# Kernel tuning notes

Hardware: AMD Instinct MI355X
Metric: run time of the kernel (lower is better)

Reference implementation:

```python
import jax, jax.numpy as jnp
import numpy as np

MAX_K = 4
KAPPA_MAX = 80.0
TEMP = 0.7

NPOINT1, NSAMPLE1 = 128, 32
NPOINT2, NSAMPLE2 = 32, 32


def _sqdist(a, b):
    # a: (B,M,3), b: (B,N,3) -> (B,M,N) squared euclidean distance
    return (jnp.sum(a * a, -1)[:, :, None] + jnp.sum(b * b, -1)[:, None, :]
            - 2.0 * jnp.einsum('bmc,bnc->bmn', a, b))


def _fps(xyz, npoint):
    # farthest point sampling, sequential over npoint (inherent recurrence)
    B, N, _ = xyz.shape
    def step(carry, _):
        dist, far = carry
        centroid = jnp.take_along_axis(xyz, far[:, None, None], axis=1)  # (B,1,3)
        d = jnp.sum((xyz - centroid) ** 2, -1)                            # (B,N)
        dist = jnp.minimum(dist, d)
        nxt = jnp.argmax(dist, -1).astype(jnp.int32)
        return (dist, nxt), far
    init = (jnp.full((B, N), 1e10, xyz.dtype), jnp.zeros((B,), jnp.int32))
    _, idx = jax.lax.scan(step, init, None, length=npoint)
    return jnp.transpose(idx)  # (B, npoint)


def _gather(x, idx):
    # x: (B,N,C), idx: (B,...) int -> (B,...,C)
    return jax.vmap(lambda xb, ib: xb[ib])(x, idx)


def _sa(xyz, feats, npoint, nsample, params, group_all=False):
    # PointNet++ set abstraction: FPS + kNN grouping + shared MLP + max-pool
    if group_all:
        new_xyz = jnp.zeros((xyz.shape[0], 1, 3), xyz.dtype)
        g = xyz[:, None]                                   # (B,1,N,3)
        if feats is not None:
            g = jnp.concatenate([g, feats[:, None]], -1)   # (B,1,N,3+C)
    else:
        fidx = _fps(xyz, npoint)                           # (B,S)
        new_xyz = _gather(xyz, fidx)                       # (B,S,3)
        d = _sqdist(new_xyz, xyz)                          # (B,S,N)
        _, nidx = jax.lax.top_k(-d, nsample)               # (B,S,K) nearest
        g = _gather(xyz, nidx) - new_xyz[:, :, None]       # relative coords
        if feats is not None:
            g = jnp.concatenate([g, _gather(feats, nidx)], -1)
    for w, b in params:                                    # shared 1x1 MLP
        g = jax.nn.relu(g @ w + b)
    return new_xyz, jnp.max(g, axis=2)                     # max over group


def _ln(x, g, b, eps=1e-5):
    m = jnp.mean(x, -1, keepdims=True)
    v = jnp.var(x, -1, keepdims=True)
    return (x - m) * jax.lax.rsqrt(v + eps) * g + b


def setup_inputs() -> dict:
    key = jax.random.key(0)
    ks = iter(jax.random.split(key, 64))
    def p(shape, s=0.05):
        return jax.random.normal(next(ks), shape, jnp.float32) * s
    d = {"xyz": jax.random.normal(next(ks), (32, 16384, 3), jnp.float32)}
    sa_dims = {"sa1": [3, 64, 64, 128], "sa2": [131, 128, 128, 256], "sa3": [259, 256, 512, 1024]}
    for name, dims in sa_dims.items():
        for i in range(3):
            d[f"{name}_w{i}"] = p((dims[i], dims[i + 1]))
            d[f"{name}_b{i}"] = jnp.zeros((dims[i + 1],), jnp.float32)
    d["fc1_w"] = p((1024, 512)); d["fc1_b"] = jnp.zeros((512,), jnp.float32)
    d["ln1_g"] = jnp.ones((512,), jnp.float32); d["ln1_b"] = jnp.zeros((512,), jnp.float32)
    d["fc2_w"] = p((512, 256)); d["fc2_b"] = jnp.zeros((256,), jnp.float32)
    d["ln2_g"] = jnp.ones((256,), jnp.float32); d["ln2_b"] = jnp.zeros((256,), jnp.float32)
    d["pi_w"] = p((256, MAX_K)); d["pi_b"] = jnp.zeros((MAX_K,), jnp.float32)
    d["mu_w"] = p((256, MAX_K * 2)); d["mu_b"] = jnp.zeros((MAX_K * 2,), jnp.float32)
    d["kappa_w"] = p((256, MAX_K)); d["kappa_b"] = jnp.zeros((MAX_K,), jnp.float32)
    return d


def reference(xyz,
              sa1_w0, sa1_b0, sa1_w1, sa1_b1, sa1_w2, sa1_b2,
              sa2_w0, sa2_b0, sa2_w1, sa2_b1, sa2_w2, sa2_b2,
              sa3_w0, sa3_b0, sa3_w1, sa3_b1, sa3_w2, sa3_b2,
              fc1_w, fc1_b, ln1_g, ln1_b, fc2_w, fc2_b, ln2_g, ln2_b,
              pi_w, pi_b, mu_w, mu_b, kappa_w, kappa_b):
    l1x, l1f = _sa(xyz, None, NPOINT1, NSAMPLE1,
                   [(sa1_w0, sa1_b0), (sa1_w1, sa1_b1), (sa1_w2, sa1_b2)])
    l2x, l2f = _sa(l1x, l1f, NPOINT2, NSAMPLE2,
                   [(sa2_w0, sa2_b0), (sa2_w1, sa2_b1), (sa2_w2, sa2_b2)])
    _, l3f = _sa(l2x, l2f, None, None,
                 [(sa3_w0, sa3_b0), (sa3_w1, sa3_b1), (sa3_w2, sa3_b2)], group_all=True)
    x = l3f.reshape(l3f.shape[0], -1)  # (B,1024)
    x = jax.nn.relu(_ln(x @ fc1_w + fc1_b, ln1_g, ln1_b))  # dropout is identity in eval
    x = jax.nn.relu(_ln(x @ fc2_w + fc2_b, ln2_g, ln2_b))
    weight = jax.nn.softmax((x @ pi_w + pi_b) / TEMP, axis=-1)
    mu_raw = (x @ mu_w + mu_b).reshape(-1, MAX_K, 2)
    nrm = jnp.linalg.norm(mu_raw, axis=-1, keepdims=True)
    mu_unit = mu_raw / jnp.maximum(nrm, 1e-4)              # F.normalize(eps=1e-4)
    c, s = mu_unit[..., 0], mu_unit[..., 1]
    n2 = jnp.sqrt(c * c + s * s)
    mask = n2 < 1e-3
    c = jnp.where(mask, 1.0, c)
    s = jnp.where(mask, 0.0, s)
    mu = jnp.arctan2(s, c)
    kappa = jnp.minimum(jax.nn.softplus(x @ kappa_w + kappa_b) + 1e-6, KAPPA_MAX)
    return mu, kappa, weight
```

## Files before the change

### kernel.cpp

```cpp
#include <hip/hip_runtime.h>
#include <math.h>

#define B 32
#define N1 16384
#define NP1 128
#define NS1 32
#define NP2 32
#define NS2 32

#define OFF_L1X   0
#define OFF_G1    12288
#define OFF_L1F   405504
#define OFF_L2X   929792
#define OFF_NIDX2 932864
#define OFF_L2F   965632
#define OFF_L3F   1227776

__global__ __launch_bounds__(1024, 1) void k_fps1(const float* __restrict__ xyz,
                                                  float* __restrict__ l1x) {
  const int b = blockIdx.x, t = threadIdx.x;
  const float* xb = xyz + (size_t)b * N1 * 3;
  float px[16], py[16], pz[16], dd[16];
#pragma unroll
  for (int j = 0; j < 16; ++j) {
    int idx = t + (j << 10);
    px[j] = xb[idx * 3 + 0]; py[j] = xb[idx * 3 + 1]; pz[j] = xb[idx * 3 + 2];
    dd[j] = 1e10f;
  }
#pragma unroll
  for (int j = 0; j < 16; ++j) {
    asm volatile("" : "+v"(px[j]), "+v"(py[j]), "+v"(pz[j]));
  }
  __shared__ unsigned long long slots[2][16];
  if (t < 16) slots[0][t] = (t == 0) ? 0xFFFFFFFFull : 0ull;
  __syncthreads();
  for (int it = 0; it < NP1; ++it) {
    unsigned long long key = slots[it & 1][0];
#pragma unroll
    for (int w = 1; w < 16; ++w) {
      unsigned long long k2 = slots[it & 1][w];
      if (k2 > key) key = k2;
    }
    const int widx = (int)(0xFFFFFFFFu - (unsigned)(key & 0xFFFFFFFFull));
    const float cx = xb[widx * 3 + 0];
    const float cy = xb[widx * 3 + 1];
    const float cz = xb[widx * 3 + 2];
    if (t == 0) {
      float* o = l1x + ((size_t)b * NP1 + it) * 3;
      o[0] = cx; o[1] = cy; o[2] = cz;
    }
    float bd = -1.f; int bj = 0;
#pragma unroll
    for (int j = 0; j < 16; ++j) {
      float dx = px[j] - cx, dy = py[j] - cy, dz = pz[j] - cz;
      float d = dx * dx + dy * dy + dz * dz;
      float nd = fminf(dd[j], d);
      dd[j] = nd;
      if (nd > bd) { bd = nd; bj = j; }
    }
    unsigned long long mykey =
        ((unsigned long long)__float_as_uint(bd) << 32) |
        (unsigned long long)(0xFFFFFFFFu - (unsigned)(t + (bj << 10)));
#pragma unroll
    for (int off = 32; off > 0; off >>= 1) {
      unsigned long long ok = __shfl_down(mykey, off);
      if (ok > mykey) mykey = ok;
    }
    if ((t & 63) == 0) slots[(it + 1) & 1][t >> 6] = mykey;
    __syncthreads();
  }
}

__device__ __forceinline__ float dist3(const float* __restrict__ xb, int idx,
                                       float cx, float cy, float cz,
                                       float& x, float& y, float& z) {
  x = xb[idx * 3 + 0]; y = xb[idx * 3 + 1]; z = xb[idx * 3 + 2];
  float dx = x - cx, dy = y - cy, dz = z - cz;
  return dx * dx + dy * dy + dz * dz;
}

#define KNN_CAP 512
#define NBIN 2048

__global__ __launch_bounds__(256) void k_knn1(const float* __restrict__ xyz,
                                              const float* __restrict__ l1x,
                                              float* __restrict__ g1) {
  const int t = threadIdx.x;
  const int b = blockIdx.x & 31;
  const int m = blockIdx.x >> 5;
  const float* xb = xyz + (size_t)b * N1 * 3;
  const float* cp = l1x + ((size_t)b * NP1 + m) * 3;
  const float cx = cp[0], cy = cp[1], cz = cp[2];

  __shared__ int hist[NBIN];
  __shared__ float cd[KNN_CAP]; __shared__ int ci[KNN_CAP];
  __shared__ float cpx[KNN_CAP], cpy[KNN_CAP], cpz[KNN_CAP];
  __shared__ int s_cnt, s_cut;
  __shared__ int wsum[4];

  for (int i = t; i < NBIN; i += 256) hist[i] = 0;
  if (t == 0) { s_cnt = 0; s_cut = NBIN - 1; }
  __syncthreads();

  for (int j = 0; j < 64; ++j) {
    float x, y, z;
    float d = dist3(xb, t + (j << 8), cx, cy, cz, x, y, z);
    atomicAdd(&hist[__float_as_uint(d) >> 20], 1);
  }
  __syncthreads();

  {
    int loc = 0;
#pragma unroll
    for (int j = 0; j < 8; ++j) loc += hist[t * 8 + j];
    int v = loc;
#pragma unroll
    for (int off = 1; off < 64; off <<= 1) {
      int u = __shfl_up(v, off);
      if ((t & 63) >= off) v += u;
    }
    if ((t & 63) == 63) wsum[t >> 6] = v;
    __syncthreads();
    int woff = 0;
    for (int w = 0; w < (t >> 6); ++w) woff += wsum[w];
    int incl = v + woff, excl = incl - loc;
    if (excl < NS1 && incl >= NS1) {
      int c = excl;
#pragma unroll
      for (int j = 0; j < 8; ++j) {
        c += hist[t * 8 + j];
        if (c >= NS1) { s_cut = t * 8 + j; break; }
      }
    }
  }
  __syncthreads();
  const unsigned cut = (unsigned)s_cut + 1u;

  for (int j = 0; j < 64; ++j) {
    float x, y, z;
    float d = dist3(xb, t + (j << 8), cx, cy, cz, x, y, z);
    if ((__float_as_uint(d) >> 20) <= cut) {
      int p = atomicAdd(&s_cnt, 1);
      if (p < KNN_CAP) { cd[p] = d; ci[p] = t + (j << 8); cpx[p] = x; cpy[p] = y; cpz[p] = z; }
    }
  }
  __syncthreads();
  const int cnt = (s_cnt < KNN_CAP) ? s_cnt : KNN_CAP;

  float* gout = g1 + ((size_t)(b * NP1 + m)) * NS1 * 3;
  for (int p = t; p < cnt; p += 256) {
    const float dp = cd[p]; const int ip = ci[p];
    int rank = 0;
    for (int q = 0; q < cnt; ++q) {
      float dq = cd[q];
      rank += (dq < dp || (dq == dp && ci[q] < ip)) ? 1 : 0;
    }
    if (rank < NS1) {
      gout[rank * 3 + 0] = cpx[p] - cx;
      gout[rank * 3 + 1] = cpy[p] - cy;
      gout[rank * 3 + 2] = cpz[p] - cz;
    }
  }
}

template <int K, int C, int TPT>
__device__ __forceinline__ void sa_layer(const float* __restrict__ W,
                                         const float* __restrict__ bias,
                                         const float* __restrict__ hin, int instride,
                                         float* __restrict__ hout,
                                         unsigned* __restrict__ om,
                                         float* __restrict__ wst, int t) {
  constexpr int CT = C / 4;
  constexpr int NT = 8 * CT;
  float acc[TPT][4][4];
  int s4[TPT], c4[TPT]; bool on[TPT];
#pragma unroll
  for (int p = 0; p < TPT; ++p) {
    int tile = t + p * 256;
    on[p] = tile < NT;
    int tl = on[p] ? tile : 0;
    s4[p] = (tl / CT) * 4; c4[p] = (tl % CT) * 4;
    float4 bb = *(const float4*)(bias + c4[p]);
#pragma unroll
    for (int i = 0; i < 4; ++i) {
      acc[p][i][0] = bb.x; acc[p][i][1] = bb.y; acc[p][i][2] = bb.z; acc[p][i][3] = bb.w;
    }
  }
  for (int k0 = 0; k0 < K; k0 += 16) {
    const int kc = (K - k0 < 16) ? (K - k0) : 16;
    __syncthreads();
    for (int i = t; i < kc * C; i += 256) wst[i] = W[k0 * C + i];
    __syncthreads();
    if (kc == 16) {
#pragma unroll
      for (int kk = 0; kk < 16; ++kk) {
#pragma unroll
        for (int p = 0; p < TPT; ++p) {
          float4 w = *(const float4*)(wst + kk * C + c4[p]);
#pragma unroll
          for (int i = 0; i < 4; ++i) {
            float a = hin[(s4[p] + i) * instride + (k0 + kk)];
            acc[p][i][0] += a * w.x; acc[p][i][1] += a * w.y;
            acc[p][i][2] += a * w.z; acc[p][i][3] += a * w.w;
          }
        }
      }
    } else {
      for (int kk = 0; kk < kc; ++kk) {
#pragma unroll
        for (int p = 0; p < TPT; ++p) {
          float4 w = *(const float4*)(wst + kk * C + c4[p]);
#pragma unroll
          for (int i = 0; i < 4; ++i) {
            float a = hin[(s4[p] + i) * instride + (k0 + kk)];
            acc[p][i][0] += a * w.x; acc[p][i][1] += a * w.y;
            acc[p][i][2] += a * w.z; acc[p][i][3] += a * w.w;
          }
        }
      }
    }
  }
#pragma unroll
  for (int p = 0; p < TPT; ++p) {
    if (!on[p]) continue;
    if (om) {
#pragma unroll
      for (int j = 0; j < 4; ++j) {
        float vm = fmaxf(fmaxf(fmaxf(acc[p][0][j], acc[p][1][j]),
                               fmaxf(acc[p][2][j], acc[p][3][j])), 0.f);
        atomicMax(&om[c4[p] + j], __float_as_uint(vm));
      }
    } else {
#pragma unroll
      for (int i = 0; i < 4; ++i)
#pragma unroll
        for (int j = 0; j < 4; ++j)
          hout[(s4[p] + i) * C + c4[p] + j] = fmaxf(acc[p][i][j], 0.f);
    }
  }
}

__global__ __launch_bounds__(256) void k_mlp1(const float* __restrict__ g1,
    const float* __restrict__ w0, const float* __restrict__ b0,
    const float* __restrict__ w1, const float* __restrict__ b1,
    const float* __restrict__ w2, const float* __restrict__ b2,
    float* __restrict__ l1f) {
  const int t = threadIdx.x;
  const int b = blockIdx.x & 31, m = blockIdx.x >> 5;
  __shared__ __align__(16) float h0[32 * 4];
  __shared__ __align__(16) float h1[32 * 64];
  __shared__ __align__(16) float h2[32 * 64];
  __shared__ __align__(16) float wst[16 * 128];
  __shared__ unsigned om[128];
  const float* gi = g1 + ((size_t)(b * NP1 + m)) * NS1 * 3;
  if (t < 96) h0[(t / 3) * 4 + (t % 3)] = gi[t];
  if (t < 128) om[t] = 0u;
  __syncthreads();
  sa_layer<3, 64, 1>(w0, b0, h0, 4, h1, nullptr, wst, t);
  sa_layer<64, 64, 1>(w1, b1, h1, 64, h2, nullptr, wst, t);
  sa_layer<64, 128, 1>(w2, b2, h2, 64, nullptr, om, wst, t);
  __syncthreads();
  if (t < 128) l1f[((size_t)(b * NP1 + m)) * 128 + t] = __uint_as_float(om[t]);
}

__global__ __launch_bounds__(128) void k_fps2(const float* __restrict__ l1x,
                                              float* __restrict__ l2x) {
  const int b = blockIdx.x, t = threadIdx.x;
  const float* xb = l1x + (size_t)b * NP1 * 3;
  float px = xb[t * 3], py = xb[t * 3 + 1], pz = xb[t * 3 + 2];
  float dd = 1e10f;
  __shared__ float swv[2]; __shared__ int swi[2];
  __shared__ float s_cx, s_cy, s_cz; __shared__ int s_far;
  if (t == 0) { s_cx = xb[0]; s_cy = xb[1]; s_cz = xb[2]; }
  __syncthreads();
  for (int it = 0; it < NP2; ++it) {
    float cx = s_cx, cy = s_cy, cz = s_cz;
    if (t == 0) {
      float* o = l2x + ((size_t)b * NP2 + it) * 3;
      o[0] = cx; o[1] = cy; o[2] = cz;
    }
    float dx = px - cx, dy = py - cy, dz = pz - cz;
    dd = fminf(dd, dx * dx + dy * dy + dz * dz);
    float bd = dd; int bi = t;
#pragma unroll
    for (int off = 32; off > 0; off >>= 1) {
      float od = __shfl_down(bd, off); int oi = __shfl_down(bi, off);
      if (od > bd || (od == bd && oi < bi)) { bd = od; bi = oi; }
    }
    if ((t & 63) == 0) { swv[t >> 6] = bd; swi[t >> 6] = bi; }
    __syncthreads();
    if (t == 0) {
      if (swv[1] > bd || (swv[1] == bd && swi[1] < bi)) bi = swi[1];
      s_far = bi;
    }
    __syncthreads();
    if (t == s_far) { s_cx = px; s_cy = py; s_cz = pz; }
    __syncthreads();
  }
}

__global__ __launch_bounds__(256) void k_knn2(const float* __restrict__ l1x,
                                              const float* __restrict__ l2x,
                                              int* __restrict__ nidx2) {
  const int b = blockIdx.x, t = threadIdx.x;
  const int lane = t & 63, wv = t >> 6;
  __shared__ float pxs[128], pys[128], pzs[128];
  if (t < 128) {
    pxs[t] = l1x[((size_t)b * NP1 + t) * 3 + 0];
    pys[t] = l1x[((size_t)b * NP1 + t) * 3 + 1];
    pzs[t] = l1x[((size_t)b * NP1 + t) * 3 + 2];
  }
  __syncthreads();
  for (int mc = wv; mc < NP2; mc += 4) {
    const float* cp = l2x + ((size_t)b * NP2 + mc) * 3;
    float cx = cp[0], cy = cp[1], cz = cp[2];
    float dx = pxs[lane] - cx, dy = pys[lane] - cy, dz = pzs[lane] - cz;
    float d0 = dx * dx + dy * dy + dz * dz;
    dx = pxs[lane + 64] - cx; dy = pys[lane + 64] - cy; dz = pzs[lane + 64] - cz;
    float d1 = dx * dx + dy * dy + dz * dz;
    int* no = nidx2 + ((size_t)b * NP2 + mc) * NS2;
    for (int it = 0; it < NS2; ++it) {
      float bv; int bi;
      if (d1 < d0) { bv = d1; bi = lane + 64; } else { bv = d0; bi = lane; }
#pragma unroll
      for (int off = 32; off > 0; off >>= 1) {
        float ov = __shfl_down(bv, off); int oi = __shfl_down(bi, off);
        if (ov < bv || (ov == bv && oi < bi)) { bv = ov; bi = oi; }
      }
      bi = __shfl(bi, 0);
      if (lane == (bi & 63)) { if (bi < 64) d0 = 1e30f; else d1 = 1e30f; }
      if (lane == 0) no[it] = bi;
    }
  }
}

__global__ __launch_bounds__(256) void k_mlp2(const float* __restrict__ l1x,
    const float* __restrict__ l2x, const float* __restrict__ l1f,
    const int* __restrict__ nidx2,
    const float* __restrict__ w0, const float* __restrict__ b0,
    const float* __restrict__ w1, const float* __restrict__ b1,
    const float* __restrict__ w2, const float* __restrict__ b2,
    float* __restrict__ l2f) {
  const int t = threadIdx.x;
  const int b = blockIdx.x & 31, mc = blockIdx.x >> 5;
  __shared__ __align__(16) float h0[32 * 132];
  __shared__ __align__(16) float h1[32 * 128];
  __shared__ __align__(16) float wst[16 * 256];
  __shared__ unsigned om[256];
  __shared__ int sni[32];
  if (t < 32) sni[t] = nidx2[((size_t)b * NP2 + mc) * NS2 + t];
  om[t] = 0u;
  __syncthreads();
  const float* l1fb = l1f + (size_t)b * NP1 * 128;
  for (int i = t; i < 32 * 128; i += 256) {
    int r = i >> 7, cc = i & 127;
    h0[r * 132 + 3 + cc] = l1fb[(size_t)sni[r] * 128 + cc];
  }
  if (t < 96) {
    int r = t / 3, ax = t - 3 * r;
    h0[r * 132 + ax] = l1x[((size_t)b * NP1 + sni[r]) * 3 + ax] -
                       l2x[((size_t)b * NP2 + mc) * 3 + ax];
  }
  __syncthreads();
  sa_layer<131, 128, 1>(w0, b0, h0, 132, h1, nullptr, wst, t);
  sa_layer<128, 128, 1>(w1, b1, h1, 128, h0, nullptr, wst, t);
  sa_layer<128, 256, 2>(w2, b2, h0, 128, nullptr, om, wst, t);
  __syncthreads();
  l2f[((size_t)(b * NP2 + mc)) * 256 + t] = __uint_as_float(om[t]);
}

__global__ __launch_bounds__(512) void k_mlp3(const float* __restrict__ l2x,
    const float* __restrict__ l2f,
    const float* __restrict__ w0, const float* __restrict__ b0,
    const float* __restrict__ w1, const float* __restrict__ b1,
    const float* __restrict__ w2, const float* __restrict__ b2,
    float* __restrict__ l3f) {
  const int t = threadIdx.x;
  const int b = blockIdx.x & 31, sg = blockIdx.x >> 5;
  __shared__ float in[4][260];
  __shared__ float h1[4][256];
  __shared__ float h2[4][512];
  for (int i = t; i < 4 * 256; i += 512) {
    int s = i >> 8, c = i & 255;
    in[s][3 + c] = l2f[((size_t)(b * NP2) + sg * 4 + s) * 256 + c];
  }
  if (t < 12) {
    int s = t / 3, ax = t - 3 * s;
    in[s][ax] = l2x[((size_t)b * NP2 + sg * 4 + s) * 3 + ax];
  }
  __syncthreads();
  if (t < 256) {
    float a0 = b0[t], a1 = a0, a2 = a0, a3 = a0;
    for (int k = 0; k < 259; ++k) {
      float w = w0[k * 256 + t];
      a0 += in[0][k] * w; a1 += in[1][k] * w; a2 += in[2][k] * w; a3 += in[3][k] * w;
    }
    h1[0][t] = fmaxf(a0, 0.f); h1[1][t] = fmaxf(a1, 0.f);
    h1[2][t] = fmaxf(a2, 0.f); h1[3][t] = fmaxf(a3, 0.f);
  }
  __syncthreads();
  {
    float a0 = b1[t], a1 = a0, a2 = a0, a3 = a0;
    for (int k = 0; k < 256; ++k) {
      float w = w1[k * 512 + t];
      a0 += h1[0][k] * w; a1 += h1[1][k] * w; a2 += h1[2][k] * w; a3 += h1[3][k] * w;
    }
    h2[0][t] = fmaxf(a0, 0.f); h2[1][t] = fmaxf(a1, 0.f);
    h2[2][t] = fmaxf(a2, 0.f); h2[3][t] = fmaxf(a3, 0.f);
  }
  __syncthreads();
  {
    float a[2][4];
#pragma unroll
    for (int p = 0; p < 2; ++p) {
      float bv = b2[t + p * 512];
      a[p][0] = bv; a[p][1] = bv; a[p][2] = bv; a[p][3] = bv;
    }
    for (int k = 0; k < 512; ++k) {
      float x0 = h2[0][k], x1 = h2[1][k], x2 = h2[2][k], x3 = h2[3][k];
      float wA = w2[k * 1024 + t];
      float wB = w2[k * 1024 + t + 512];
      a[0][0] += x0 * wA; a[0][1] += x1 * wA; a[0][2] += x2 * wA; a[0][3] += x3 * wA;
      a[1][0] += x0 * wB; a[1][1] += x1 * wB; a[1][2] += x2 * wB; a[1][3] += x3 * wB;
    }
#pragma unroll
    for (int p = 0; p < 2; ++p) {
      float vm = fmaxf(fmaxf(fmaxf(a[p][0], a[p][1]), fmaxf(a[p][2], a[p][3])), 0.f);
      atomicMax((unsigned*)l3f + (size_t)b * 1024 + t + p * 512, __float_as_uint(vm));
    }
  }
}

__global__ __launch_bounds__(256) void k_head(const float* __restrict__ l3f,
    const float* __restrict__ fc1w, const float* __restrict__ fc1b,
    const float* __restrict__ lg1, const float* __restrict__ lb1,
    const float* __restrict__ fc2w, const float* __restrict__ fc2b,
    const float* __restrict__ lg2, const float* __restrict__ lb2,
    const float* __restrict__ piw, const float* __restrict__ pib,
    const float* __restrict__ muw, const float* __restrict__ mub,
    const float* __restrict__ kw, const float* __restrict__ kb,
    float* __restrict__ out) {
  const int b = blockIdx.x, t = threadIdx.x;
  __shared__ float x[1024], x1[512], x2[256];
  __shared__ float red[8];
  __shared__ float hv[16];
  for (int i = t; i < 1024; i += 256) x[i] = l3f[(size_t)b * 1024 + i];
  __syncthreads();
  float a0 = fc1b[t], a1 = fc1b[t + 256];
  for (int k = 0; k < 1024; ++k) {
    float xv = x[k];
    a0 += xv * fc1w[k * 512 + t];
    a1 += xv * fc1w[k * 512 + t + 256];
  }
  {
    float s = a0 + a1, ss = a0 * a0 + a1 * a1;
#pragma unroll
    for (int off = 32; off > 0; off >>= 1) { s += __shfl_down(s, off); ss += __shfl_down(ss, off); }
    if ((t & 63) == 0) { red[t >> 6] = s; red[4 + (t >> 6)] = ss; }
    __syncthreads();
    if (t == 0) {
      float S = red[0] + red[1] + red[2] + red[3];
      float SS = red[4] + red[5] + red[6] + red[7];
      float mean = S / 512.f;
      red[0] = mean; red[4] = SS / 512.f - mean * mean;
    }
    __syncthreads();
    float mean = red[0], var = red[4];
    float rs = rsqrtf(var + 1e-5f);
    x1[t]       = fmaxf((a0 - mean) * rs * lg1[t] + lb1[t], 0.f);
    x1[t + 256] = fmaxf((a1 - mean) * rs * lg1[t + 256] + lb1[t + 256], 0.f);
  }
  __syncthreads();
  float a = fc2b[t];
  for (int k = 0; k < 512; ++k) a += x1[k] * fc2w[k * 256 + t];
  {
    float s = a, ss = a * a;
#pragma unroll
    for (int off = 32; off > 0; off >>= 1) { s += __shfl_down(s, off); ss += __shfl_down(ss, off); }
    if ((t & 63) == 0) { red[t >> 6] = s; red[4 + (t >> 6)] = ss; }
    __syncthreads();
    if (t == 0) {
      float S = red[0] + red[1] + red[2] + red[3];
      float SS = red[4] + red[5] + red[6] + red[7];
      float mean = S / 256.f;
      red[0] = mean; red[4] = SS / 256.f - mean * mean;
    }
    __syncthreads();
    float mean = red[0], var = red[4];
    x2[t] = fmaxf((a - mean) * rsqrtf(var + 1e-5f) * lg2[t] + lb2[t], 0.f);
  }
  __syncthreads();
  if (t < 16) {
    const float* W; const float* bb; int c; int C;
    if (t < 4)        { W = piw; bb = pib; c = t;      C = 4; }
    else if (t < 12)  { W = muw; bb = mub; c = t - 4;  C = 8; }
    else              { W = kw;  bb = kb;  c = t - 12; C = 4; }
    float acc = bb[c];
    for (int k = 0; k < 256; ++k) acc += x2[k] * W[k * C + c];
    hv[t] = acc;
  }
  __syncthreads();
  if (t == 0) {
    float z[4], mx = -1e30f;
#pragma unroll
    for (int i = 0; i < 4; ++i) { z[i] = hv[i] / 0.7f; mx = fmaxf(mx, z[i]); }
    float e[4], sum = 0.f;
#pragma unroll
    for (int i = 0; i < 4; ++i) { e[i] = expf(z[i] - mx); sum += e[i]; }
#pragma unroll
    for (int k = 0; k < 4; ++k) {
      float c0 = hv[4 + 2 * k], s0 = hv[4 + 2 * k + 1];
      float nr = sqrtf(c0 * c0 + s0 * s0);
      float den = fmaxf(nr, 1e-4f);
      float cu = c0 / den, su = s0 / den;
      float n2 = sqrtf(cu * cu + su * su);
      if (n2 < 1e-3f) { cu = 1.f; su = 0.f; }
      out[b * 4 + k] = atan2f(su, cu);
      float zk = hv[12 + k];
      float sp = fmaxf(zk, 0.f) + log1pf(expf(-fabsf(zk)));
      out[128 + b * 4 + k] = fminf(sp + 1e-6f, 80.f);
      out[256 + b * 4 + k] = e[k] / sum;
    }
  }
}

extern "C" void kernel_launch(void* const* d_in, const int* in_sizes, int n_in,
                              void* d_out, int out_size, void* d_ws, size_t ws_size,
                              hipStream_t stream) {
  const float* xyz  = (const float*)d_in[0];
  const float* s1w0 = (const float*)d_in[1];  const float* s1b0 = (const float*)d_in[2];
  const float* s1w1 = (const float*)d_in[3];  const float* s1b1 = (const float*)d_in[4];
  const float* s1w2 = (const float*)d_in[5];  const float* s1b2 = (const float*)d_in[6];
  const float* s2w0 = (const float*)d_in[7];  const float* s2b0 = (const float*)d_in[8];
  const float* s2w1 = (const float*)d_in[9];  const float* s2b1 = (const float*)d_in[10];
  const float* s2w2 = (const float*)d_in[11]; const float* s2b2 = (const float*)d_in[12];
  const float* s3w0 = (const float*)d_in[13]; const float* s3b0 = (const float*)d_in[14];
  const float* s3w1 = (const float*)d_in[15]; const float* s3b1 = (const float*)d_in[16];
  const float* s3w2 = (const float*)d_in[17]; const float* s3b2 = (const float*)d_in[18];
  const float* fc1w = (const float*)d_in[19]; const float* fc1b = (const float*)d_in[20];
  const float* lg1  = (const float*)d_in[21]; const float* lb1  = (const float*)d_in[22];
  const float* fc2w = (const float*)d_in[23]; const float* fc2b = (const float*)d_in[24];
  const float* lg2  = (const float*)d_in[25]; const float* lb2  = (const float*)d_in[26];
  const float* piw  = (const float*)d_in[27]; const float* pib  = (const float*)d_in[28];
  const float* muw  = (const float*)d_in[29]; const float* mub  = (const float*)d_in[30];
  const float* kw   = (const float*)d_in[31]; const float* kb   = (const float*)d_in[32];

  float* ws   = (float*)d_ws;
  float* l1x  = ws + OFF_L1X;
  float* g1   = ws + OFF_G1;
  float* l1f  = ws + OFF_L1F;
  float* l2x  = ws + OFF_L2X;
  int*   nid2 = (int*)(ws + OFF_NIDX2);
  float* l2f  = ws + OFF_L2F;
  float* l3f  = ws + OFF_L3F;
  float* out  = (float*)d_out;

  hipMemsetAsync(l3f, 0, (size_t)B * 1024 * sizeof(float), stream);
  k_fps1<<<B, 1024, 0, stream>>>(xyz, l1x);
  k_knn1<<<B * NP1, 256, 0, stream>>>(xyz, l1x, g1);
  k_mlp1<<<B * NP1, 256, 0, stream>>>(g1, s1w0, s1b0, s1w1, s1b1, s1w2, s1b2, l1f);
  k_fps2<<<B, 128, 0, stream>>>(l1x, l2x);
  k_knn2<<<B, 256, 0, stream>>>(l1x, l2x, nid2);
  k_mlp2<<<B * NP2, 256, 0, stream>>>(l1x, l2x, l1f, nid2,
                                      s2w0, s2b0, s2w1, s2b1, s2w2, s2b2, l2f);
  k_mlp3<<<B * 8, 512, 0, stream>>>(l2x, l2f, s3w0, s3b0, s3w1, s3b1, s3w2, s3b2, l3f);
  k_head<<<B, 256, 0, stream>>>(l3f, fc1w, fc1b, lg1, lb1, fc2w, fc2b, lg2, lb2,
                                piw, pib, muw, mub, kw, kb, out);
}
```

Before: 939.3 us.

## Stage FPS1 points in LDS and global SoA buffer instead of registers

The first farthest-point-sampling kernel stops holding all 16 points per thread in registers. A quarter of the points go to shared memory as float4 SoA, and the other three quarters go to a global scratch area that is reread every iteration. Each thread now owns 4 consecutive points per group, so the point index encoding changes to match. The aim is to cut register pressure and improve coalescing. The cost is LDS traffic plus repeated global (likely L2-resident) loads on every one of the 128 sequential iterations. The scratch area reuses the g1 workspace region, which is only written later by knn1.

```diff
diff --git a/kernel.cpp b/kernel.cpp
--- a/kernel.cpp
+++ b/kernel.cpp
@@ -15,25 +15,52 @@
 #define OFF_NIDX2 932864
 #define OFF_L2F   965632
 #define OFF_L3F   1227776
+#define OFF_STAGE 12288
+#define STAGE_PER_B 36864
+
+#define FPS_UPD(j, XX, YY, ZZ) {                                        \
+    float dx = (XX) - cx, dy = (YY) - cy, dz = (ZZ) - cz;               \
+    float d = dx * dx + dy * dy + dz * dz;                              \
+    float nd = fminf(dd[j], d);                                         \
+    dd[j] = nd;                                                         \
+    if (nd > bd) { bd = nd; bj = (j); }                                 \
+  }
+#define FPS_UPD4(jb, X, Y, Z)                                           \
+    FPS_UPD((jb) + 0, X.x, Y.x, Z.x)                                    \
+    FPS_UPD((jb) + 1, X.y, Y.y, Z.y)                                    \
+    FPS_UPD((jb) + 2, X.z, Y.z, Z.z)                                    \
+    FPS_UPD((jb) + 3, X.w, Y.w, Z.w)
 
 __global__ __launch_bounds__(1024, 1) void k_fps1(const float* __restrict__ xyz,
-                                                  float* __restrict__ l1x) {
+                                                  float* __restrict__ l1x,
+                                                  float* __restrict__ stage) {
   const int b = blockIdx.x, t = threadIdx.x;
   const float* xb = xyz + (size_t)b * N1 * 3;
-  float px[16], py[16], pz[16], dd[16];
-#pragma unroll
-  for (int j = 0; j < 16; ++j) {
-    int idx = t + (j << 10);
-    px[j] = xb[idx * 3 + 0]; py[j] = xb[idx * 3 + 1]; pz[j] = xb[idx * 3 + 2];
-    dd[j] = 1e10f;
-  }
-#pragma unroll
-  for (int j = 0; j < 16; ++j) {
-    asm volatile("" : "+v"(px[j]), "+v"(py[j]), "+v"(pz[j]));
-  }
+  float* sb = stage + (size_t)b * STAGE_PER_B;
+  __shared__ float4 sx[1024], sy[1024], sz[1024];
   __shared__ unsigned long long slots[2][16];
+
+#pragma unroll
+  for (int g = 0; g < 4; ++g) {
+    const int q = t + (g << 10);
+    const float* p = xb + (size_t)q * 12;
+    float4 X = make_float4(p[0], p[3], p[6], p[9]);
+    float4 Y = make_float4(p[1], p[4], p[7], p[10]);
+    float4 Z = make_float4(p[2], p[5], p[8], p[11]);
+    if (g == 0) { sx[t] = X; sy[t] = Y; sz[t] = Z; }
+    else {
+      float* gb = sb + (size_t)(g - 1) * 12288;
+      ((float4*)gb)[t] = X;
+      ((float4*)(gb + 4096))[t] = Y;
+      ((float4*)(gb + 8192))[t] = Z;
+    }
+  }
+  float dd[16];
+#pragma unroll
+  for (int j = 0; j < 16; ++j) dd[j] = 1e10f;
   if (t < 16) slots[0][t] = (t == 0) ? 0xFFFFFFFFull : 0ull;
   __syncthreads();
+
   for (int it = 0; it < NP1; ++it) {
     unsigned long long key = slots[it & 1][0];
 #pragma unroll
@@ -50,17 +77,22 @@
       o[0] = cx; o[1] = cy; o[2] = cz;
     }
     float bd = -1.f; int bj = 0;
-#pragma unroll
-    for (int j = 0; j < 16; ++j) {
-      float dx = px[j] - cx, dy = py[j] - cy, dz = pz[j] - cz;
-      float d = dx * dx + dy * dy + dz * dz;
-      float nd = fminf(dd[j], d);
-      dd[j] = nd;
-      if (nd > bd) { bd = nd; bj = j; }
-    }
+    {
+      float4 X = sx[t], Y = sy[t], Z = sz[t];
+      FPS_UPD4(0, X, Y, Z)
+    }
+#pragma unroll
+    for (int g = 1; g < 4; ++g) {
+      const float* gb = sb + (size_t)(g - 1) * 12288;
+      float4 X = ((const float4*)gb)[t];
+      float4 Y = ((const float4*)(gb + 4096))[t];
+      float4 Z = ((const float4*)(gb + 8192))[t];
+      FPS_UPD4(4 * g, X, Y, Z)
+    }
+    const unsigned gidx = 4u * (unsigned)(t + ((bj >> 2) << 10)) + (unsigned)(bj & 3);
     unsigned long long mykey =
         ((unsigned long long)__float_as_uint(bd) << 32) |
-        (unsigned long long)(0xFFFFFFFFu - (unsigned)(t + (bj << 10)));
+        (unsigned long long)(0xFFFFFFFFu - gidx);
 #pragma unroll
     for (int off = 32; off > 0; off >>= 1) {
       unsigned long long ok = __shfl_down(mykey, off);
@@ -553,10 +585,11 @@
   int*   nid2 = (int*)(ws + OFF_NIDX2);
   float* l2f  = ws + OFF_L2F;
   float* l3f  = ws + OFF_L3F;
+  float* stage = ws + OFF_STAGE;
   float* out  = (float*)d_out;
 
   hipMemsetAsync(l3f, 0, (size_t)B * 1024 * sizeof(float), stream);
-  k_fps1<<<B, 1024, 0, stream>>>(xyz, l1x);
+  k_fps1<<<B, 1024, 0, stream>>>(xyz, l1x, stage);
   k_knn1<<<B * NP1, 256, 0, stream>>>(xyz, l1x, g1);
   k_mlp1<<<B * NP1, 256, 0, stream>>>(g1, s1w0, s1b0, s1w1, s1b1, s1w2, s1b2, l1f);
   k_fps2<<<B, 128, 0, stream>>>(l1x, l2x);
```

Measured after the change: 990.6 us. 5.5% more time.
